# Performance work log

Measured on AMD Instinct MI355X. Metric: run time of the kernel, lower is better.

## Reference

```python
import jax, jax.numpy as jnp
import numpy as np

B, Lq, Skv = 4, 512, 4096
INPUT_DIM, QUERY_DIM, HIDDEN_DIM, CROSS_HEAD = 256, 256, 512, 8
MID_DIM = HIDDEN_DIM // 2          # 256, V/output width
HEAD_DIM = QUERY_DIM // CROSS_HEAD # 32
VHEAD_DIM = MID_DIM // CROSS_HEAD  # 32


def setup_inputs() -> dict:
    key = jax.random.key(0)
    ks = jax.random.split(key, 8)
    query = jax.random.normal(ks[0], (B, Lq, INPUT_DIM), dtype=jnp.float32)
    key_value = jax.random.normal(ks[1], (B, Skv, INPUT_DIM), dtype=jnp.float32)
    mask = jax.random.randint(ks[2], (B, Skv), 0, 2, dtype=jnp.int32)
    s = 1.0 / np.sqrt(INPUT_DIM)
    Wq = jax.random.normal(ks[3], (INPUT_DIM, QUERY_DIM), dtype=jnp.float32) * s
    Wk = jax.random.normal(ks[4], (INPUT_DIM, QUERY_DIM), dtype=jnp.float32) * s
    Wv = jax.random.normal(ks[5], (INPUT_DIM, MID_DIM), dtype=jnp.float32) * s
    Wo = jax.random.normal(ks[6], (MID_DIM, HIDDEN_DIM), dtype=jnp.float32) * (1.0 / np.sqrt(MID_DIM))
    bo = jax.random.normal(ks[7], (HIDDEN_DIM,), dtype=jnp.float32) * 0.01
    return {"query": query, "key_value": key_value, "mask": mask,
            "Wq": Wq, "Wk": Wk, "Wv": Wv, "Wo": Wo, "bo": bo}


def reference(query, key_value, mask, Wq, Wk, Wv, Wo, bo):
    scale = jnp.asarray(np.sqrt(HEAD_DIM), dtype=query.dtype)
    # Projections
    Q = (query @ Wq).reshape(B, Lq, CROSS_HEAD, HEAD_DIM).transpose(0, 2, 1, 3)      # [B,H,Lq,dh]
    K = (key_value @ Wk).reshape(B, Skv, CROSS_HEAD, HEAD_DIM).transpose(0, 2, 1, 3)  # [B,H,Skv,dh]
    V = (key_value @ Wv).reshape(B, Skv, CROSS_HEAD, VHEAD_DIM).transpose(0, 2, 1, 3) # [B,H,Skv,dv]
    # Scaled dot-product energy
    energy = jnp.einsum('bhqd,bhkd->bhqk', Q, K) / scale                              # [B,H,Lq,Skv]
    # Key-padding mask broadcast over heads and query positions
    keep = (mask[:, None, None, :] != 0)                                              # [B,1,1,Skv]
    energy = jnp.where(keep, energy, -jnp.inf)
    attention = jax.nn.softmax(energy, axis=-1)
    # dropout_ratio = 0 -> identity
    x = jnp.einsum('bhqk,bhkd->bhqd', attention, V)                                   # [B,H,Lq,dv]
    x = x.transpose(0, 2, 1, 3).reshape(B, Lq, MID_DIM)
    x = x @ Wo + bo                                                                   # [B,Lq,HIDDEN_DIM]
    return (x, attention, energy)
```

## Files before the change

### kernel.cpp

```cpp
#include <hip/hip_runtime.h>
#include <cstdint>
#include <cmath>

#define INV_SCALE 0.17677669529663687f
#define NEG_BIG   (-1e30f)

__device__ __forceinline__ void unpack8(float* d, float4 a, float4 b) {
  d[0]=a.x; d[1]=a.y; d[2]=a.z; d[3]=a.w; d[4]=b.x; d[5]=b.y; d[6]=b.z; d[7]=b.w;
}

__device__ __forceinline__ void gemm_body(const float* __restrict__ A,
                                          const float* __restrict__ W,
                                          const float* __restrict__ bias,
                                          float* __restrict__ C,
                                          int m0, int n0, int N) {
  __shared__ float At[16][132];
  __shared__ float Ws[16][132];
  const int t  = threadIdx.x;
  const int mg = t & 15;
  const int ng = t >> 4;
  const int am  = t & 127;
  const int ak8 = (t >> 7) << 3;
  const int wk  = t >> 4;
  const int wn8 = (t & 15) << 3;

  float acc[8][8];
#pragma unroll
  for (int i = 0; i < 8; ++i)
#pragma unroll
    for (int j = 0; j < 8; ++j) acc[i][j] = 0.f;

  float4 a0 = *(const float4*)&A[(size_t)(m0 + am) * 256 + ak8];
  float4 a1 = *(const float4*)&A[(size_t)(m0 + am) * 256 + ak8 + 4];
  float4 w0 = *(const float4*)&W[(size_t)wk * N + n0 + wn8];
  float4 w1 = *(const float4*)&W[(size_t)wk * N + n0 + wn8 + 4];

  for (int k0 = 0; k0 < 256; k0 += 16) {
    __syncthreads();
    At[ak8 + 0][am] = a0.x; At[ak8 + 1][am] = a0.y;
    At[ak8 + 2][am] = a0.z; At[ak8 + 3][am] = a0.w;
    At[ak8 + 4][am] = a1.x; At[ak8 + 5][am] = a1.y;
    At[ak8 + 6][am] = a1.z; At[ak8 + 7][am] = a1.w;
    *(float4*)&Ws[wk][wn8]     = w0;
    *(float4*)&Ws[wk][wn8 + 4] = w1;
    __syncthreads();
    if (k0 + 16 < 256) {
      a0 = *(const float4*)&A[(size_t)(m0 + am) * 256 + k0 + 16 + ak8];
      a1 = *(const float4*)&A[(size_t)(m0 + am) * 256 + k0 + 16 + ak8 + 4];
      w0 = *(const float4*)&W[(size_t)(k0 + 16 + wk) * N + n0 + wn8];
      w1 = *(const float4*)&W[(size_t)(k0 + 16 + wk) * N + n0 + wn8 + 4];
    }
#pragma unroll 4
    for (int kk = 0; kk < 16; ++kk) {
      float av[8], wv[8];
      unpack8(av, *(const float4*)&At[kk][mg * 8], *(const float4*)&At[kk][mg * 8 + 4]);
      unpack8(wv, *(const float4*)&Ws[kk][ng * 8], *(const float4*)&Ws[kk][ng * 8 + 4]);
#pragma unroll
      for (int i = 0; i < 8; ++i)
#pragma unroll
        for (int j = 0; j < 8; ++j) acc[i][j] += av[i] * wv[j];
    }
  }

#pragma unroll
  for (int i = 0; i < 8; ++i) {
    float4 o0, o1;
    if (bias) {
      o0.x = acc[i][0] + bias[n0 + ng * 8 + 0];
      o0.y = acc[i][1] + bias[n0 + ng * 8 + 1];
      o0.z = acc[i][2] + bias[n0 + ng * 8 + 2];
      o0.w = acc[i][3] + bias[n0 + ng * 8 + 3];
      o1.x = acc[i][4] + bias[n0 + ng * 8 + 4];
      o1.y = acc[i][5] + bias[n0 + ng * 8 + 5];
      o1.z = acc[i][6] + bias[n0 + ng * 8 + 6];
      o1.w = acc[i][7] + bias[n0 + ng * 8 + 7];
    } else {
      o0.x = acc[i][0]; o0.y = acc[i][1]; o0.z = acc[i][2]; o0.w = acc[i][3];
      o1.x = acc[i][4]; o1.y = acc[i][5]; o1.z = acc[i][6]; o1.w = acc[i][7];
    }
    float* dst = &C[(size_t)(m0 + mg * 8 + i) * N + n0 + ng * 8];
    *(float4*)dst       = o0;
    *(float4*)(dst + 4) = o1;
  }
}

__global__ __launch_bounds__(256) void proj3_kernel(
    const float* __restrict__ q_in, const float* __restrict__ kv_in,
    const float* __restrict__ Wq, const float* __restrict__ Wk,
    const float* __restrict__ Wv, float* __restrict__ Qp,
    float* __restrict__ Kp, float* __restrict__ Vp) {
  const float* A; const float* W; float* C; int M;
  if (blockIdx.z == 0)      { A = q_in;  W = Wq; C = Qp; M = 2048;  }
  else if (blockIdx.z == 1) { A = kv_in; W = Wk; C = Kp; M = 16384; }
  else                      { A = kv_in; W = Wv; C = Vp; M = 16384; }
  int m0 = blockIdx.x * 128;
  if (m0 >= M) return;
  gemm_body(A, W, nullptr, C, m0, blockIdx.y * 128, 256);
}

__global__ __launch_bounds__(256) void out_proj_kernel(
    const float* __restrict__ xmid, const float* __restrict__ Wo,
    const float* __restrict__ bo, float* __restrict__ out) {
  gemm_body(xmid, Wo, bo, out, blockIdx.x * 128, blockIdx.y * 128, 512);
}

__global__ __launch_bounds__(256) void energy_kernel(
    const float* __restrict__ Qp, const float* __restrict__ Kp,
    const int* __restrict__ mask, float* __restrict__ Eout,
    float* __restrict__ mrow, float* __restrict__ rrow) {
  __shared__ float Qt[32][68];
  __shared__ float Kt[32][260];
  __shared__ float redM[32][65];
  __shared__ float redS[32][65];
  __shared__ int   msk[256];
  const int t  = threadIdx.x;
  const int bh = blockIdx.y, b = bh >> 3, h = bh & 7;
  const int q0 = blockIdx.x * 64;
  const int mg = t & 7;
  const int kg = t >> 3;

  {
    int m = t >> 2, i8 = (t & 3) << 3;
    const float* src = &Qp[(size_t)(b * 512 + q0 + m) * 256 + h * 32 + i8];
    float4 v0 = *(const float4*)src;
    float4 v1 = *(const float4*)(src + 4);
    Qt[i8 + 0][m] = v0.x; Qt[i8 + 1][m] = v0.y; Qt[i8 + 2][m] = v0.z; Qt[i8 + 3][m] = v0.w;
    Qt[i8 + 4][m] = v1.x; Qt[i8 + 5][m] = v1.y; Qt[i8 + 6][m] = v1.z; Qt[i8 + 7][m] = v1.w;
  }

  float m_run = NEG_BIG, s_run = 0.f;

  float kr[32];
  {
    const float* src = &Kp[(size_t)(b * 4096 + t) * 256 + h * 32];
#pragma unroll
    for (int u = 0; u < 8; ++u) *(float4*)&kr[u * 4] = *(const float4*)(src + u * 4);
  }
  int mv = mask[b * 4096 + t];

  for (int kc = 0; kc < 4096; kc += 256) {
    __syncthreads();
#pragma unroll
    for (int i = 0; i < 32; ++i) Kt[i][t] = kr[i];
    msk[t] = mv;
    __syncthreads();
    if (kc + 256 < 4096) {
      const float* src = &Kp[(size_t)(b * 4096 + kc + 256 + t) * 256 + h * 32];
#pragma unroll
      for (int u = 0; u < 8; ++u) *(float4*)&kr[u * 4] = *(const float4*)(src + u * 4);
      mv = mask[b * 4096 + kc + 256 + t];
    }

    float e[8][8];
#pragma unroll
    for (int i = 0; i < 8; ++i)
#pragma unroll
      for (int j = 0; j < 8; ++j) e[i][j] = 0.f;

#pragma unroll 4
    for (int i = 0; i < 32; ++i) {
      float qa[8], ka[8];
      unpack8(qa, *(const float4*)&Qt[i][mg * 8], *(const float4*)&Qt[i][mg * 8 + 4]);
      unpack8(ka, *(const float4*)&Kt[i][kg * 8], *(const float4*)&Kt[i][kg * 8 + 4]);
#pragma unroll
      for (int qi = 0; qi < 8; ++qi)
#pragma unroll
        for (int kj = 0; kj < 8; ++kj) e[qi][kj] += qa[qi] * ka[kj];
    }

    int km[8];
#pragma unroll
    for (int j = 0; j < 8; ++j) km[j] = msk[kg * 8 + j];

#pragma unroll
    for (int iq = 0; iq < 8; ++iq) {
      int q = mg * 8 + iq;
      float v[8];
#pragma unroll
      for (int j = 0; j < 8; ++j) {
        float ev = e[iq][j] * INV_SCALE;
        v[j] = (km[j] != 0) ? ev : NEG_BIG;
      }
      size_t base = ((size_t)(bh * 512 + q0 + q)) * 4096 + kc + kg * 8;
      *(float4*)&Eout[base]     = make_float4(v[0], v[1], v[2], v[3]);
      *(float4*)&Eout[base + 4] = make_float4(v[4], v[5], v[6], v[7]);
      float mx = fmaxf(fmaxf(fmaxf(v[0], v[1]), fmaxf(v[2], v[3])),
                       fmaxf(fmaxf(v[4], v[5]), fmaxf(v[6], v[7])));
      float ss = expf(v[0] - mx) + expf(v[1] - mx) + expf(v[2] - mx) + expf(v[3] - mx)
               + expf(v[4] - mx) + expf(v[5] - mx) + expf(v[6] - mx) + expf(v[7] - mx);
      redM[kg][q] = mx;
      redS[kg][q] = ss;
    }
    __syncthreads();
    if (t < 64) {
      float M = NEG_BIG;
#pragma unroll
      for (int g = 0; g < 32; ++g) M = fmaxf(M, redM[g][t]);
      float S = 0.f;
#pragma unroll
      for (int g = 0; g < 32; ++g) S += redS[g][t] * expf(redM[g][t] - M);
      float nm = fmaxf(m_run, M);
      s_run = s_run * expf(m_run - nm) + S * expf(M - nm);
      m_run = nm;
    }
  }
  if (t < 64) {
    mrow[bh * 512 + q0 + t] = m_run;
    rrow[bh * 512 + q0 + t] = 1.0f / s_run;
  }
}

__global__ __launch_bounds__(256) void attn_pv_kernel(
    const float* __restrict__ Ein, const float* __restrict__ Vp,
    const float* __restrict__ mrow, const float* __restrict__ rrow,
    float* __restrict__ Aout, float* __restrict__ xmid) {
  __shared__ float At4[4][32][68];
  __shared__ float Vs[128][36];
  __shared__ float mq[64], rq[64];
  __shared__ float pvred[64 * 33];
  const int t  = threadIdx.x;
  const int bh = blockIdx.y, b = bh >> 3, h = bh & 7;
  const int q0 = blockIdx.x * 64;
  const int qg = t & 7;
  const int dg = (t >> 3) & 3;
  const int ks = t >> 5;
  const int vk = t >> 1, vi = (t & 1) << 4;
  const int aq = t >> 5, an = t & 31;

  if (t < 64) {
    mq[t] = mrow[bh * 512 + q0 + t];
    rq[t] = rrow[bh * 512 + q0 + t];
  }

  float acc[8][8];
#pragma unroll
  for (int i = 0; i < 8; ++i)
#pragma unroll
    for (int j = 0; j < 8; ++j) acc[i][j] = 0.f;

  float4 vr0, vr1, vr2, vr3;
  {
    const float* src = &Vp[(size_t)(b * 4096 + vk) * 256 + h * 32 + vi];
    vr0 = *(const float4*)(src);     vr1 = *(const float4*)(src + 4);
    vr2 = *(const float4*)(src + 8); vr3 = *(const float4*)(src + 12);
  }
  __syncthreads();

  for (int kc = 0; kc < 4096; kc += 128) {
    *(float4*)&Vs[vk][vi]      = vr0;
    *(float4*)&Vs[vk][vi + 4]  = vr1;
    *(float4*)&Vs[vk][vi + 8]  = vr2;
    *(float4*)&Vs[vk][vi + 12] = vr3;
#pragma unroll
    for (int p = 0; p < 8; ++p) {
      int q = aq + p * 8;
      size_t base = ((size_t)(bh * 512 + q0 + q)) * 4096 + kc + an * 4;
      float4 ev = *(const float4*)&Ein[base];
      float m = mq[q], r = rq[q];
      float4 av;
      av.x = expf(ev.x - m) * r;
      av.y = expf(ev.y - m) * r;
      av.z = expf(ev.z - m) * r;
      av.w = expf(ev.w - m) * r;
      *(float4*)&Aout[base] = av;
      At4[0][an][q] = av.x;
      At4[1][an][q] = av.y;
      At4[2][an][q] = av.z;
      At4[3][an][q] = av.w;
    }
    __syncthreads();
    if (kc + 128 < 4096) {
      const float* src = &Vp[(size_t)(b * 4096 + kc + 128 + vk) * 256 + h * 32 + vi];
      vr0 = *(const float4*)(src);     vr1 = *(const float4*)(src + 4);
      vr2 = *(const float4*)(src + 8); vr3 = *(const float4*)(src + 12);
    }
#pragma unroll 4
    for (int kk = 0; kk < 16; ++kk) {
      int k  = ks * 16 + kk;
      int m_ = ks * 4 + (kk >> 2);
      int j_ = kk & 3;
      float a[8], v[8];
      unpack8(a, *(const float4*)&At4[j_][m_][qg * 8], *(const float4*)&At4[j_][m_][qg * 8 + 4]);
      unpack8(v, *(const float4*)&Vs[k][dg * 8],       *(const float4*)&Vs[k][dg * 8 + 4]);
#pragma unroll
      for (int i = 0; i < 8; ++i)
#pragma unroll
        for (int j = 0; j < 8; ++j) acc[i][j] += a[i] * v[j];
    }
    __syncthreads();
  }

  for (int s = 0; s < 8; ++s) {
    if (ks == s) {
#pragma unroll
      for (int i = 0; i < 8; ++i)
#pragma unroll
        for (int j = 0; j < 8; ++j) {
          int q = qg * 8 + i, d = dg * 8 + j;
          if (s == 0) pvred[q * 33 + d] = acc[i][j];
          else        pvred[q * 33 + d] += acc[i][j];
        }
    }
    __syncthreads();
  }
  for (int idx = t; idx < 2048; idx += 256) {
    int q = idx >> 5, d = idx & 31;
    xmid[((size_t)(b * 512) + q0 + q) * 256 + h * 32 + d] = pvred[q * 33 + d];
  }
}

extern "C" void kernel_launch(void* const* d_in, const int* in_sizes, int n_in,
                              void* d_out, int out_size, void* d_ws, size_t ws_size,
                              hipStream_t stream) {
  const float* query     = (const float*)d_in[0];
  const float* key_value = (const float*)d_in[1];
  const int*   mask      = (const int*)  d_in[2];
  const float* Wq        = (const float*)d_in[3];
  const float* Wk        = (const float*)d_in[4];
  const float* Wv        = (const float*)d_in[5];
  const float* Wo        = (const float*)d_in[6];
  const float* bo        = (const float*)d_in[7];

  float* out        = (float*)d_out;
  float* x_out      = out;
  float* attn_out   = out + 1048576;
  float* energy_out = out + 68157440;

  float* ws   = (float*)d_ws;
  float* Qp   = ws;
  float* Kp   = ws + 524288;
  float* Vp   = ws + 4718592;
  float* xmid = ws + 8912896;
  float* mrow = ws + 9437184;
  float* rrow = ws + 9453568;

  proj3_kernel<<<dim3(128, 2, 3), 256, 0, stream>>>(query, key_value, Wq, Wk, Wv,
                                                    Qp, Kp, Vp);
  energy_kernel<<<dim3(8, 32), 256, 0, stream>>>(Qp, Kp, mask, energy_out, mrow, rrow);
  attn_pv_kernel<<<dim3(8, 32), 256, 0, stream>>>(energy_out, Vp, mrow, rrow,
                                                  attn_out, xmid);
  out_proj_kernel<<<dim3(16, 4), 256, 0, stream>>>(xmid, Wo, bo, x_out);
}
```

Before: 887.3 us.

## Split KV across blocks, shrink tiles, add stats merge, prefetch energy

```diff
diff --git a/kernel.cpp b/kernel.cpp
--- a/kernel.cpp
+++ b/kernel.cpp
@@ -9,76 +9,60 @@
   d[0]=a.x; d[1]=a.y; d[2]=a.z; d[3]=a.w; d[4]=b.x; d[5]=b.y; d[6]=b.z; d[7]=b.w;
 }
 
-__device__ __forceinline__ void gemm_body(const float* __restrict__ A,
-                                          const float* __restrict__ W,
-                                          const float* __restrict__ bias,
-                                          float* __restrict__ C,
-                                          int m0, int n0, int N) {
-  __shared__ float At[16][132];
+__device__ __forceinline__ void gemm_64x128(const float* __restrict__ A,
+                                            const float* __restrict__ W,
+                                            float* __restrict__ C,
+                                            int m0, int n0, int N) {
+  __shared__ float At[16][68];
   __shared__ float Ws[16][132];
-  const int t  = threadIdx.x;
-  const int mg = t & 15;
-  const int ng = t >> 4;
-  const int am  = t & 127;
-  const int ak8 = (t >> 7) << 3;
+  const int t   = threadIdx.x;
+  const int mg  = t & 15;
+  const int ng  = t >> 4;
+  const int am  = t & 63;
+  const int ak4 = (t >> 6) << 2;
   const int wk  = t >> 4;
   const int wn8 = (t & 15) << 3;
 
-  float acc[8][8];
-#pragma unroll
-  for (int i = 0; i < 8; ++i)
+  float acc[4][8];
+#pragma unroll
+  for (int i = 0; i < 4; ++i)
 #pragma unroll
     for (int j = 0; j < 8; ++j) acc[i][j] = 0.f;
 
-  float4 a0 = *(const float4*)&A[(size_t)(m0 + am) * 256 + ak8];
-  float4 a1 = *(const float4*)&A[(size_t)(m0 + am) * 256 + ak8 + 4];
+  float4 a0 = *(const float4*)&A[(size_t)(m0 + am) * 256 + ak4];
   float4 w0 = *(const float4*)&W[(size_t)wk * N + n0 + wn8];
   float4 w1 = *(const float4*)&W[(size_t)wk * N + n0 + wn8 + 4];
 
   for (int k0 = 0; k0 < 256; k0 += 16) {
     __syncthreads();
-    At[ak8 + 0][am] = a0.x; At[ak8 + 1][am] = a0.y;
-    At[ak8 + 2][am] = a0.z; At[ak8 + 3][am] = a0.w;
-    At[ak8 + 4][am] = a1.x; At[ak8 + 5][am] = a1.y;
-    At[ak8 + 6][am] = a1.z; At[ak8 + 7][am] = a1.w;
+    At[ak4 + 0][am] = a0.x; At[ak4 + 1][am] = a0.y;
+    At[ak4 + 2][am] = a0.z; At[ak4 + 3][am] = a0.w;
     *(float4*)&Ws[wk][wn8]     = w0;
     *(float4*)&Ws[wk][wn8 + 4] = w1;
     __syncthreads();
     if (k0 + 16 < 256) {
-      a0 = *(const float4*)&A[(size_t)(m0 + am) * 256 + k0 + 16 + ak8];
-      a1 = *(const float4*)&A[(size_t)(m0 + am) * 256 + k0 + 16 + ak8 + 4];
+      a0 = *(const float4*)&A[(size_t)(m0 + am) * 256 + k0 + 16 + ak4];
       w0 = *(const float4*)&W[(size_t)(k0 + 16 + wk) * N + n0 + wn8];
       w1 = *(const float4*)&W[(size_t)(k0 + 16 + wk) * N + n0 + wn8 + 4];
     }
 #pragma unroll 4
     for (int kk = 0; kk < 16; ++kk) {
-      float av[8], wv[8];
-      unpack8(av, *(const float4*)&At[kk][mg * 8], *(const float4*)&At[kk][mg * 8 + 4]);
+      float av[4], wv[8];
+      *(float4*)av = *(const float4*)&At[kk][mg * 4];
       unpack8(wv, *(const float4*)&Ws[kk][ng * 8], *(const float4*)&Ws[kk][ng * 8 + 4]);
 #pragma unroll
-      for (int i = 0; i < 8; ++i)
+      for (int i = 0; i < 4; ++i)
 #pragma unroll
         for (int j = 0; j < 8; ++j) acc[i][j] += av[i] * wv[j];
     }
   }
 
 #pragma unroll
-  for (int i = 0; i < 8; ++i) {
+  for (int i = 0; i < 4; ++i) {
     float4 o0, o1;
-    if (bias) {
-      o0.x = acc[i][0] + bias[n0 + ng * 8 + 0];
-      o0.y = acc[i][1] + bias[n0 + ng * 8 + 1];
-      o0.z = acc[i][2] + bias[n0 + ng * 8 + 2];
-      o0.w = acc[i][3] + bias[n0 + ng * 8 + 3];
-      o1.x = acc[i][4] + bias[n0 + ng * 8 + 4];
-      o1.y = acc[i][5] + bias[n0 + ng * 8 + 5];
-      o1.z = acc[i][6] + bias[n0 + ng * 8 + 6];
-      o1.w = acc[i][7] + bias[n0 + ng * 8 + 7];
-    } else {
-      o0.x = acc[i][0]; o0.y = acc[i][1]; o0.z = acc[i][2]; o0.w = acc[i][3];
-      o1.x = acc[i][4]; o1.y = acc[i][5]; o1.z = acc[i][6]; o1.w = acc[i][7];
-    }
-    float* dst = &C[(size_t)(m0 + mg * 8 + i) * N + n0 + ng * 8];
+    o0.x = acc[i][0]; o0.y = acc[i][1]; o0.z = acc[i][2]; o0.w = acc[i][3];
+    o1.x = acc[i][4]; o1.y = acc[i][5]; o1.z = acc[i][6]; o1.w = acc[i][7];
+    float* dst = &C[(size_t)(m0 + mg * 4 + i) * N + n0 + ng * 8];
     *(float4*)dst       = o0;
     *(float4*)(dst + 4) = o1;
   }
@@ -93,29 +77,82 @@
   if (blockIdx.z == 0)      { A = q_in;  W = Wq; C = Qp; M = 2048;  }
   else if (blockIdx.z == 1) { A = kv_in; W = Wk; C = Kp; M = 16384; }
   else                      { A = kv_in; W = Wv; C = Vp; M = 16384; }
-  int m0 = blockIdx.x * 128;
+  int m0 = blockIdx.x * 64;
   if (m0 >= M) return;
-  gemm_body(A, W, nullptr, C, m0, blockIdx.y * 128, 256);
+  gemm_64x128(A, W, C, m0, blockIdx.y * 128, 256);
 }
 
 __global__ __launch_bounds__(256) void out_proj_kernel(
     const float* __restrict__ xmid, const float* __restrict__ Wo,
     const float* __restrict__ bo, float* __restrict__ out) {
-  gemm_body(xmid, Wo, bo, out, blockIdx.x * 128, blockIdx.y * 128, 512);
+  __shared__ float At[16][68];
+  __shared__ float Ws[16][68];
+  const int t   = threadIdx.x;
+  const int mg  = t & 15;
+  const int ng  = t >> 4;
+  const int am  = t & 63;
+  const int ak4 = (t >> 6) << 2;
+  const int wk  = t >> 4;
+  const int wn4 = (t & 15) << 2;
+  const int m0 = blockIdx.x * 64, n0 = blockIdx.y * 64;
+
+  float acc[4][4];
+#pragma unroll
+  for (int i = 0; i < 4; ++i)
+#pragma unroll
+    for (int j = 0; j < 4; ++j) acc[i][j] = 0.f;
+
+  float4 a0 = *(const float4*)&xmid[(size_t)(m0 + am) * 256 + ak4];
+  float4 w0 = *(const float4*)&Wo[(size_t)wk * 512 + n0 + wn4];
+
+  for (int k0 = 0; k0 < 256; k0 += 16) {
+    __syncthreads();
+    At[ak4 + 0][am] = a0.x; At[ak4 + 1][am] = a0.y;
+    At[ak4 + 2][am] = a0.z; At[ak4 + 3][am] = a0.w;
+    *(float4*)&Ws[wk][wn4] = w0;
+    __syncthreads();
+    if (k0 + 16 < 256) {
+      a0 = *(const float4*)&xmid[(size_t)(m0 + am) * 256 + k0 + 16 + ak4];
+      w0 = *(const float4*)&Wo[(size_t)(k0 + 16 + wk) * 512 + n0 + wn4];
+    }
+#pragma unroll 4
+    for (int kk = 0; kk < 16; ++kk) {
+      float av[4], wv[4];
+      *(float4*)av = *(const float4*)&At[kk][mg * 4];
+      *(float4*)wv = *(const float4*)&Ws[kk][ng * 4];
+#pragma unroll
+      for (int i = 0; i < 4; ++i)
+#pragma unroll
+        for (int j = 0; j < 4; ++j) acc[i][j] += av[i] * wv[j];
+    }
+  }
+
+#pragma unroll
+  for (int i = 0; i < 4; ++i) {
+    float4 o;
+    o.x = acc[i][0] + bo[n0 + ng * 4 + 0];
+    o.y = acc[i][1] + bo[n0 + ng * 4 + 1];
+    o.z = acc[i][2] + bo[n0 + ng * 4 + 2];
+    o.w = acc[i][3] + bo[n0 + ng * 4 + 3];
+    *(float4*)&out[(size_t)(m0 + mg * 4 + i) * 512 + n0 + ng * 4] = o;
+  }
 }
 
 __global__ __launch_bounds__(256) void energy_kernel(
     const float* __restrict__ Qp, const float* __restrict__ Kp,
     const int* __restrict__ mask, float* __restrict__ Eout,
-    float* __restrict__ mrow, float* __restrict__ rrow) {
+    float* __restrict__ pm, float* __restrict__ ps) {
   __shared__ float Qt[32][68];
   __shared__ float Kt[32][260];
   __shared__ float redM[32][65];
   __shared__ float redS[32][65];
+  __shared__ float redM2[4][65];
+  __shared__ float redS2[4][65];
   __shared__ int   msk[256];
   const int t  = threadIdx.x;
   const int bh = blockIdx.y, b = bh >> 3, h = bh & 7;
   const int q0 = blockIdx.x * 64;
+  const int kbase = blockIdx.z * 1024;
   const int mg = t & 7;
   const int kg = t >> 3;
 
@@ -132,23 +169,23 @@
 
   float kr[32];
   {
-    const float* src = &Kp[(size_t)(b * 4096 + t) * 256 + h * 32];
+    const float* src = &Kp[(size_t)(b * 4096 + kbase + t) * 256 + h * 32];
 #pragma unroll
     for (int u = 0; u < 8; ++u) *(float4*)&kr[u * 4] = *(const float4*)(src + u * 4);
   }
-  int mv = mask[b * 4096 + t];
-
-  for (int kc = 0; kc < 4096; kc += 256) {
+  int mv = mask[b * 4096 + kbase + t];
+
+  for (int kc = 0; kc < 1024; kc += 256) {
     __syncthreads();
 #pragma unroll
     for (int i = 0; i < 32; ++i) Kt[i][t] = kr[i];
     msk[t] = mv;
     __syncthreads();
-    if (kc + 256 < 4096) {
-      const float* src = &Kp[(size_t)(b * 4096 + kc + 256 + t) * 256 + h * 32];
+    if (kc + 256 < 1024) {
+      const float* src = &Kp[(size_t)(b * 4096 + kbase + kc + 256 + t) * 256 + h * 32];
 #pragma unroll
       for (int u = 0; u < 8; ++u) *(float4*)&kr[u * 4] = *(const float4*)(src + u * 4);
-      mv = mask[b * 4096 + kc + 256 + t];
+      mv = mask[b * 4096 + kbase + kc + 256 + t];
     }
 
     float e[8][8];
@@ -181,53 +218,77 @@
         float ev = e[iq][j] * INV_SCALE;
         v[j] = (km[j] != 0) ? ev : NEG_BIG;
       }
-      size_t base = ((size_t)(bh * 512 + q0 + q)) * 4096 + kc + kg * 8;
+      size_t base = ((size_t)(bh * 512 + q0 + q)) * 4096 + kbase + kc + kg * 8;
       *(float4*)&Eout[base]     = make_float4(v[0], v[1], v[2], v[3]);
       *(float4*)&Eout[base + 4] = make_float4(v[4], v[5], v[6], v[7]);
       float mx = fmaxf(fmaxf(fmaxf(v[0], v[1]), fmaxf(v[2], v[3])),
                        fmaxf(fmaxf(v[4], v[5]), fmaxf(v[6], v[7])));
-      float ss = expf(v[0] - mx) + expf(v[1] - mx) + expf(v[2] - mx) + expf(v[3] - mx)
-               + expf(v[4] - mx) + expf(v[5] - mx) + expf(v[6] - mx) + expf(v[7] - mx);
+      float ss = __expf(v[0] - mx) + __expf(v[1] - mx) + __expf(v[2] - mx) + __expf(v[3] - mx)
+               + __expf(v[4] - mx) + __expf(v[5] - mx) + __expf(v[6] - mx) + __expf(v[7] - mx);
       redM[kg][q] = mx;
       redS[kg][q] = ss;
     }
     __syncthreads();
+    {
+      int r = t & 63, sub = t >> 6;
+      float M = NEG_BIG;
+#pragma unroll
+      for (int g = sub * 8; g < sub * 8 + 8; ++g) M = fmaxf(M, redM[g][r]);
+      float S = 0.f;
+#pragma unroll
+      for (int g = sub * 8; g < sub * 8 + 8; ++g) S += redS[g][r] * __expf(redM[g][r] - M);
+      redM2[sub][r] = M;
+      redS2[sub][r] = S;
+    }
+    __syncthreads();
     if (t < 64) {
       float M = NEG_BIG;
 #pragma unroll
-      for (int g = 0; g < 32; ++g) M = fmaxf(M, redM[g][t]);
+      for (int s = 0; s < 4; ++s) M = fmaxf(M, redM2[s][t]);
       float S = 0.f;
 #pragma unroll
-      for (int g = 0; g < 32; ++g) S += redS[g][t] * expf(redM[g][t] - M);
+      for (int s = 0; s < 4; ++s) S += redS2[s][t] * __expf(redM2[s][t] - M);
       float nm = fmaxf(m_run, M);
-      s_run = s_run * expf(m_run - nm) + S * expf(M - nm);
+      s_run = s_run * __expf(m_run - nm) + S * __expf(M - nm);
       m_run = nm;
     }
   }
   if (t < 64) {
-    mrow[bh * 512 + q0 + t] = m_run;
-    rrow[bh * 512 + q0 + t] = 1.0f / s_run;
-  }
+    pm[(size_t)blockIdx.z * 16384 + bh * 512 + q0 + t] = m_run;
+    ps[(size_t)blockIdx.z * 16384 + bh * 512 + q0 + t] = s_run;
+  }
+}
+
+__global__ __launch_bounds__(256) void merge_stats_kernel(
+    const float* __restrict__ pm, const float* __restrict__ ps,
+    float* __restrict__ mrow, float* __restrict__ rrow) {
+  int r = blockIdx.x * 256 + threadIdx.x;
+  float m0 = pm[r], m1 = pm[16384 + r], m2 = pm[32768 + r], m3 = pm[49152 + r];
+  float M = fmaxf(fmaxf(m0, m1), fmaxf(m2, m3));
+  float S = ps[r]         * __expf(m0 - M) + ps[16384 + r] * __expf(m1 - M)
+          + ps[32768 + r] * __expf(m2 - M) + ps[49152 + r] * __expf(m3 - M);
+  mrow[r] = M;
+  rrow[r] = 1.0f / S;
 }
 
 __global__ __launch_bounds__(256) void attn_pv_kernel(
     const float* __restrict__ Ein, const float* __restrict__ Vp,
     const float* __restrict__ mrow, const float* __restrict__ rrow,
     float* __restrict__ Aout, float* __restrict__ xmid) {
-  __shared__ float At4[4][32][68];
+  __shared__ float At4[4][32][36];
   __shared__ float Vs[128][36];
-  __shared__ float mq[64], rq[64];
-  __shared__ float pvred[64 * 33];
+  __shared__ float mq[32], rq[32];
+  __shared__ float pvred[32 * 33];
   const int t  = threadIdx.x;
   const int bh = blockIdx.y, b = bh >> 3, h = bh & 7;
-  const int q0 = blockIdx.x * 64;
-  const int qg = t & 7;
-  const int dg = (t >> 3) & 3;
-  const int ks = t >> 5;
+  const int q0 = blockIdx.x * 32;
+  const int qg = t & 3;
+  const int dg = (t >> 2) & 3;
+  const int ks = t >> 4;
   const int vk = t >> 1, vi = (t & 1) << 4;
   const int aq = t >> 5, an = t & 31;
 
-  if (t < 64) {
+  if (t < 32) {
     mq[t] = mrow[bh * 512 + q0 + t];
     rq[t] = rrow[bh * 512 + q0 + t];
   }
@@ -244,6 +305,11 @@
     vr0 = *(const float4*)(src);     vr1 = *(const float4*)(src + 4);
     vr2 = *(const float4*)(src + 8); vr3 = *(const float4*)(src + 12);
   }
+  float4 evp[4];
+#pragma unroll
+  for (int p = 0; p < 4; ++p)
+    evp[p] = *(const float4*)&Ein[((size_t)(bh * 512 + q0 + aq + p * 8)) * 4096 + an * 4];
+
   __syncthreads();
 
   for (int kc = 0; kc < 4096; kc += 128) {
@@ -252,16 +318,16 @@
     *(float4*)&Vs[vk][vi + 8]  = vr2;
     *(float4*)&Vs[vk][vi + 12] = vr3;
 #pragma unroll
-    for (int p = 0; p < 8; ++p) {
+    for (int p = 0; p < 4; ++p) {
       int q = aq + p * 8;
       size_t base = ((size_t)(bh * 512 + q0 + q)) * 4096 + kc + an * 4;
-      float4 ev = *(const float4*)&Ein[base];
+      float4 ev = evp[p];
       float m = mq[q], r = rq[q];
       float4 av;
-      av.x = expf(ev.x - m) * r;
-      av.y = expf(ev.y - m) * r;
-      av.z = expf(ev.z - m) * r;
-      av.w = expf(ev.w - m) * r;
+      av.x = __expf(ev.x - m) * r;
+      av.y = __expf(ev.y - m) * r;
+      av.z = __expf(ev.z - m) * r;
+      av.w = __expf(ev.w - m) * r;
       *(float4*)&Aout[base] = av;
       At4[0][an][q] = av.x;
       At4[1][an][q] = av.y;
@@ -273,12 +339,16 @@
       const float* src = &Vp[(size_t)(b * 4096 + kc + 128 + vk) * 256 + h * 32 + vi];
       vr0 = *(const float4*)(src);     vr1 = *(const float4*)(src + 4);
       vr2 = *(const float4*)(src + 8); vr3 = *(const float4*)(src + 12);
+#pragma unroll
+      for (int p = 0; p < 4; ++p)
+        evp[p] = *(const float4*)&Ein[((size_t)(bh * 512 + q0 + aq + p * 8)) * 4096
+                                      + kc + 128 + an * 4];
     }
 #pragma unroll 4
-    for (int kk = 0; kk < 16; ++kk) {
-      int k  = ks * 16 + kk;
-      int m_ = ks * 4 + (kk >> 2);
-      int j_ = kk & 3;
+    for (int kk = 0; kk < 8; ++kk) {
+      int k  = ks * 8 + kk;
+      int m_ = k >> 2;
+      int j_ = k & 3;
       float a[8], v[8];
       unpack8(a, *(const float4*)&At4[j_][m_][qg * 8], *(const float4*)&At4[j_][m_][qg * 8 + 4]);
       unpack8(v, *(const float4*)&Vs[k][dg * 8],       *(const float4*)&Vs[k][dg * 8 + 4]);
@@ -290,7 +360,7 @@
     __syncthreads();
   }
 
-  for (int s = 0; s < 8; ++s) {
+  for (int s = 0; s < 16; ++s) {
     if (ks == s) {
 #pragma unroll
       for (int i = 0; i < 8; ++i)
@@ -303,7 +373,7 @@
     }
     __syncthreads();
   }
-  for (int idx = t; idx < 2048; idx += 256) {
+  for (int idx = t; idx < 1024; idx += 256) {
     int q = idx >> 5, d = idx & 31;
     xmid[((size_t)(b * 512) + q0 + q) * 256 + h * 32 + d] = pvred[q * 33 + d];
   }
@@ -331,13 +401,16 @@
   float* Kp   = ws + 524288;
   float* Vp   = ws + 4718592;
   float* xmid = ws + 8912896;
+  float* pm   = xmid;
+  float* ps   = xmid + 65536;
   float* mrow = ws + 9437184;
   float* rrow = ws + 9453568;
 
-  proj3_kernel<<<dim3(128, 2, 3), 256, 0, stream>>>(query, key_value, Wq, Wk, Wv,
+  proj3_kernel<<<dim3(256, 2, 3), 256, 0, stream>>>(query, key_value, Wq, Wk, Wv,
                                                     Qp, Kp, Vp);
-  energy_kernel<<<dim3(8, 32), 256, 0, stream>>>(Qp, Kp, mask, energy_out, mrow, rrow);
-  attn_pv_kernel<<<dim3(8, 32), 256, 0, stream>>>(energy_out, Vp, mrow, rrow,
-                                                  attn_out, xmid);
-  out_proj_kernel<<<dim3(16, 4), 256, 0, stream>>>(xmid, Wo, bo, x_out);
-}
+  energy_kernel<<<dim3(8, 32, 4), 256, 0, stream>>>(Qp, Kp, mask, energy_out, pm, ps);
+  merge_stats_kernel<<<dim3(64), 256, 0, stream>>>(pm, ps, mrow, rrow);
+  attn_pv_kernel<<<dim3(16, 32), 256, 0, stream>>>(energy_out, Vp, mrow, rrow,
+                                                   attn_out, xmid);
+  out_proj_kernel<<<dim3(32, 8), 256, 0, stream>>>(xmid, Wo, bo, x_out);
+}
```

Result: faster. 788.3 us (-11.2%).
